# Kernel optimization log

Hardware: AMD Instinct MI355X
Metric: run time of the kernel (lower is better)

## Reference

```python
import jax, jax.numpy as jnp
import numpy as np

N_NODES = 100000
N_EDGES = 1600000
N_GRAPHS = 2000
IN_DIM, HID, OUT_DIM, N_CLS = 6, 256, 128, 60
EPS = 1e-5


def setup_inputs() -> dict:
    key = jax.random.key(0)
    ks = jax.random.split(key, 16)
    def lin(k, i, o):
        s = 1.0 / np.sqrt(i)
        k1, k2 = jax.random.split(k)
        return (jax.random.uniform(k1, (i, o), jnp.float32, -s, s),
                jax.random.uniform(k2, (o,), jnp.float32, -s, s))
    W_emb, b_emb = lin(ks[0], IN_DIM, HID)
    Wc1, bc1 = lin(ks[1], HID, HID)
    W2, b2 = lin(ks[2], HID, HID)
    Wc2, bc2 = lin(ks[3], HID, HID)
    W3, b3 = lin(ks[4], HID, OUT_DIM)
    Wcls, bcls = lin(ks[5], OUT_DIM, N_CLS)
    return {
        'node_features': jax.random.normal(ks[6], (N_NODES, IN_DIM), jnp.float32),
        'src': jax.random.randint(ks[7], (N_EDGES,), 0, N_NODES, jnp.int32),
        'dst': jax.random.randint(ks[8], (N_EDGES,), 0, N_NODES, jnp.int32),
        'graph_ids': jnp.sort(jax.random.randint(ks[9], (N_NODES,), 0, N_GRAPHS, jnp.int32)),
        'W_emb': W_emb, 'b_emb': b_emb,
        'Wc1': Wc1, 'bc1': bc1,
        'g1': jnp.ones((HID,), jnp.float32), 'be1': jnp.zeros((HID,), jnp.float32),
        'W2': W2, 'b2': b2,
        'Wc2': Wc2, 'bc2': bc2,
        'g2': jnp.ones((HID,), jnp.float32), 'be2': jnp.zeros((HID,), jnp.float32),
        'W3': W3, 'b3': b3,
        'Wcls': Wcls, 'bcls': bcls,
    }


def _graph_conv(x, W, b, src, dst, dout_isqrt, din_isqrt):
    # DGL GraphConv, norm='both': msg = x_src * dout^-1/2, sum to dst, * din^-1/2, then W, b
    m = x[src] * dout_isqrt[src][:, None]            # [E, H]
    agg = jax.ops.segment_sum(m, dst, num_segments=N_NODES)
    agg = agg * din_isqrt[:, None]
    return agg @ W + b


def _bn(h, g, b):
    # BatchNorm1d, training mode: batch stats over node dim, biased variance
    mu = jnp.mean(h, axis=0)
    var = jnp.mean(jnp.square(h - mu), axis=0)
    return (h - mu) * jax.lax.rsqrt(var + EPS) * g + b


def reference(node_features, src, dst, graph_ids, W_emb, b_emb, Wc1, bc1, g1, be1,
              W2, b2, Wc2, bc2, g2, be2, W3, b3, Wcls, bcls):
    ones_e = jnp.ones((N_EDGES,), jnp.float32)
    dout = jax.ops.segment_sum(ones_e, src, num_segments=N_NODES)
    din = jax.ops.segment_sum(ones_e, dst, num_segments=N_NODES)
    dout_isqrt = jnp.where(dout > 0, jax.lax.rsqrt(jnp.maximum(dout, 1.0)), 0.0)
    din_isqrt = jnp.where(din > 0, jax.lax.rsqrt(jnp.maximum(din, 1.0)), 0.0)

    x = node_features @ W_emb + b_emb                              # [N, H]
    h = x + _graph_conv(x, Wc1, bc1, src, dst, dout_isqrt, din_isqrt)
    h = jax.nn.relu(_bn(h, g1, be1))
    h = h @ W2 + b2
    h = x + _graph_conv(h, Wc2, bc2, src, dst, dout_isqrt, din_isqrt)
    h = jax.nn.relu(_bn(h, g2, be2))
    h = h @ W3 + b3                                                # [N, OUT_DIM]

    # dgl.mean_nodes: per-graph mean of h
    sums = jax.ops.segment_sum(h, graph_ids, num_segments=N_GRAPHS)
    cnts = jax.ops.segment_sum(jnp.ones((N_NODES,), jnp.float32), graph_ids, num_segments=N_GRAPHS)
    y = sums / jnp.maximum(cnts, 1.0)[:, None]                     # [G, OUT_DIM]
    label = y @ Wcls + bcls                                        # [G, N_CLS]
    return h, label
```

## Files before the change

kernel.cpp:

```cpp
#include <hip/hip_runtime.h>

#define NNODES 100000
#define MPAD   100032
#define NEDGES 1600000
#define NGRAPHS 2000
#define HID 256
#define OUTD 128
#define NCLS 60
#define BN_EPS 1e-5f
#define NROWBLK 1563
#define NSCANBLK 98
#define REDBLK 32

typedef __attribute__((ext_vector_type(8))) short bf16x8;
typedef __attribute__((ext_vector_type(4))) float f32x4;

__device__ __forceinline__ float b2f(unsigned short b) {
    unsigned int u = ((unsigned int)b) << 16;
    return __builtin_bit_cast(float, u);
}
__device__ __forceinline__ unsigned short f2b(float f) {
    unsigned int u = __builtin_bit_cast(unsigned int, f);
    u = (u + 0x7FFFu + ((u >> 16) & 1u)) >> 16;
    return (unsigned short)u;
}

__global__ void k_zero_int(int* __restrict__ p, int n) {
    int i = blockIdx.x * blockDim.x + threadIdx.x;
    if (i < n) p[i] = 0;
}

__global__ void k_deg(const int* __restrict__ src, const int* __restrict__ dst,
                      int* __restrict__ dout, int* __restrict__ din) {
    int e = blockIdx.x * blockDim.x + threadIdx.x;
    if (e < NEDGES) {
        atomicAdd(&dout[src[e]], 1);
        atomicAdd(&din[dst[e]], 1);
    }
}

__global__ void k_isqrt(const int* __restrict__ dout, const int* __restrict__ din,
                        float* __restrict__ dos, float* __restrict__ dis) {
    int i = blockIdx.x * blockDim.x + threadIdx.x;
    if (i < NNODES) {
        int a = dout[i], b = din[i];
        dos[i] = a > 0 ? 1.0f / sqrtf((float)a) : 0.0f;
        dis[i] = b > 0 ? 1.0f / sqrtf((float)b) : 0.0f;
    }
}

__global__ void k_blk_sum(const int* __restrict__ deg, int* __restrict__ bsum) {
    __shared__ int red[256];
    int blk = blockIdx.x, tid = threadIdx.x;
    int base = blk * 1024;
    int s = 0;
#pragma unroll
    for (int j = 0; j < 4; ++j) {
        int i = base + tid + j * 256;
        if (i < NNODES) s += deg[i];
    }
    red[tid] = s;
    __syncthreads();
    for (int off = 128; off > 0; off >>= 1) {
        if (tid < off) red[tid] += red[tid + off];
        __syncthreads();
    }
    if (tid == 0) bsum[blk] = red[0];
}

__global__ void k_scan_bsum(int* __restrict__ bsum) {
    if (threadIdx.x == 0) {
        int acc = 0;
        for (int i = 0; i < NSCANBLK; ++i) { int v = bsum[i]; bsum[i] = acc; acc += v; }
    }
}

__global__ void k_scan_local(const int* __restrict__ deg, const int* __restrict__ bsum,
                             int* __restrict__ row_ptr, int* __restrict__ cursor) {
    __shared__ int buf[1024];
    int blk = blockIdx.x, tid = threadIdx.x;
    int i = blk * 1024 + tid;
    int v = (i < NNODES) ? deg[i] : 0;
    buf[tid] = v;
    __syncthreads();
    for (int off = 1; off < 1024; off <<= 1) {
        int t = (tid >= off) ? buf[tid - off] : 0;
        __syncthreads();
        buf[tid] += t;
        __syncthreads();
    }
    int inc = buf[tid] + bsum[blk];
    if (i < NNODES) { row_ptr[i + 1] = inc; cursor[i] = inc - v; }
    if (i == 0) row_ptr[0] = 0;
}

__global__ void k_scatter(const int* __restrict__ src, const int* __restrict__ dst,
                          const float* __restrict__ dos, int* __restrict__ cursor,
                          int2* __restrict__ csr_ew) {
    int e = blockIdx.x * blockDim.x + threadIdx.x;
    if (e < NEDGES) {
        int s = src[e], d = dst[e];
        int pos = atomicAdd(&cursor[d], 1);
        csr_ew[pos] = make_int2(s, __float_as_int(dos[s]));
    }
}

__global__ void k_wconv(const float* __restrict__ W, unsigned short* __restrict__ Wt,
                        int K, int N) {
    int idx = blockIdx.x * 256 + threadIdx.x;
    if (idx >= N * K) return;
    int n = idx / K, k = idx - n * K;
    Wt[idx] = f2b(W[(size_t)k * N + n]);
}

__global__ void k_small_mm(const float* __restrict__ Wemb, const float* __restrict__ bemb,
                           const float* __restrict__ Wc1, float* __restrict__ M1,
                           float* __restrict__ v1) {
    int c = threadIdx.x;
    int bi = blockIdx.x;
    float acc = 0.f;
    if (bi < 6) {
        for (int k = 0; k < HID; ++k) acc = fmaf(Wemb[bi * HID + k], Wc1[k * HID + c], acc);
        M1[bi * HID + c] = acc;
    } else {
        for (int k = 0; k < HID; ++k) acc = fmaf(bemb[k], Wc1[k * HID + c], acc);
        v1[c] = acc;
    }
}

__global__ void k_agg6(const int* __restrict__ row_ptr, const int2* __restrict__ csr_ew,
                       const float* __restrict__ nf,
                       float* __restrict__ t6, float* __restrict__ u1) {
    int n = blockIdx.x * blockDim.x + threadIdx.x;
    if (n >= NNODES) return;
    float a0 = 0, a1 = 0, a2 = 0, a3 = 0, a4 = 0, a5 = 0, au = 0;
    int s = row_ptr[n], e = row_ptr[n + 1];
    int i = s;
    for (; i + 2 <= e; i += 2) {
        int2 g0 = csr_ew[i], g1 = csr_ew[i + 1];
        float w0 = __int_as_float(g0.y), w1 = __int_as_float(g1.y);
        const float* p0 = nf + (size_t)g0.x * 6;
        const float* p1 = nf + (size_t)g1.x * 6;
        a0 = fmaf(w0, p0[0], a0); a1 = fmaf(w0, p0[1], a1); a2 = fmaf(w0, p0[2], a2);
        a3 = fmaf(w0, p0[3], a3); a4 = fmaf(w0, p0[4], a4); a5 = fmaf(w0, p0[5], a5);
        au += w0;
        a0 = fmaf(w1, p1[0], a0); a1 = fmaf(w1, p1[1], a1); a2 = fmaf(w1, p1[2], a2);
        a3 = fmaf(w1, p1[3], a3); a4 = fmaf(w1, p1[4], a4); a5 = fmaf(w1, p1[5], a5);
        au += w1;
    }
    for (; i < e; ++i) {
        int2 g0 = csr_ew[i];
        float w = __int_as_float(g0.y);
        const float* p = nf + (size_t)g0.x * 6;
        a0 = fmaf(w, p[0], a0); a1 = fmaf(w, p[1], a1); a2 = fmaf(w, p[2], a2);
        a3 = fmaf(w, p[3], a3); a4 = fmaf(w, p[4], a4); a5 = fmaf(w, p[5], a5);
        au += w;
    }
    float* t = t6 + (size_t)n * 6;
    t[0] = a0; t[1] = a1; t[2] = a2; t[3] = a3; t[4] = a4; t[5] = a5;
    u1[n] = au;
}

__global__ __launch_bounds__(256) void k_layer1(
    const float* __restrict__ nf, const float* __restrict__ Wemb, const float* __restrict__ bemb,
    const float* __restrict__ M1, const float* __restrict__ v1, const float* __restrict__ bc1,
    const float* __restrict__ t6, const float* __restrict__ u1, const float* __restrict__ dis,
    unsigned short* __restrict__ H, float* __restrict__ psum, float* __restrict__ psq) {
    __shared__ float s_nf[64][6];
    __shared__ float s_t6[64][6];
    __shared__ float s_u[64];
    __shared__ float s_r[64];
    int blk = blockIdx.x;
    int n0 = blk * 64;
    int tid = threadIdx.x;
    for (int t = tid; t < 384; t += 256) {
        int nl = t / 6, i = t % 6;
        int n = n0 + nl;
        s_nf[nl][i] = (n < NNODES) ? nf[(size_t)n * 6 + i] : 0.f;
        s_t6[nl][i] = (n < NNODES) ? t6[(size_t)n * 6 + i] : 0.f;
    }
    if (tid < 64) {
        int n = n0 + tid;
        s_u[tid] = (n < NNODES) ? u1[n] : 0.f;
        s_r[tid] = (n < NNODES) ? dis[n] : 0.f;
    }
    int c = tid;
    float wc[6], mc[6];
#pragma unroll
    for (int i = 0; i < 6; ++i) { wc[i] = Wemb[i * HID + c]; mc[i] = M1[i * HID + c]; }
    float v1c = v1[c];
    float bsum = bemb[c] + bc1[c];
    __syncthreads();
    float ps = 0.f, pq = 0.f;
    int nmax = min(64, NNODES - n0);
    for (int nl = 0; nl < nmax; ++nl) {
        float nfd = 0.f, td = 0.f;
#pragma unroll
        for (int i = 0; i < 6; ++i) {
            nfd = fmaf(s_nf[nl][i], wc[i], nfd);
            td = fmaf(s_t6[nl][i], mc[i], td);
        }
        float val = nfd + s_r[nl] * (td + s_u[nl] * v1c) + bsum;
        H[(size_t)(n0 + nl) * HID + c] = f2b(val);
        ps += val;
        pq = fmaf(val, val, pq);
    }
    for (int nl = nmax; nl < 64; ++nl) H[(size_t)(n0 + nl) * HID + c] = 0;
    psum[blk * HID + c] = ps;
    psq[blk * HID + c] = pq;
}

__global__ void k_bn_part(const float* __restrict__ psum, const float* __restrict__ psq,
                          double* __restrict__ tmp) {
    int c = threadIdx.x;
    int s = blockIdx.x;
    double a = 0.0, b = 0.0;
    for (int bb = s; bb < NROWBLK; bb += REDBLK) {
        a += psum[bb * HID + c];
        b += psq[bb * HID + c];
    }
    tmp[s * HID + c] = a;
    tmp[(REDBLK + s) * HID + c] = b;
}

__global__ void k_bn_final(const double* __restrict__ tmp, const float* __restrict__ g,
                           const float* __restrict__ be, float* __restrict__ scale,
                           float* __restrict__ shift) {
    int c = threadIdx.x;
    double s = 0.0, q = 0.0;
    for (int i = 0; i < REDBLK; ++i) { s += tmp[i * HID + c]; q += tmp[(REDBLK + i) * HID + c]; }
    double mu = s / (double)NNODES;
    double var = q / (double)NNODES - mu * mu;
    if (var < 0.0) var = 0.0;
    double inv = 1.0 / sqrt(var + (double)BN_EPS);
    float sc = (float)((double)g[c] * inv);
    scale[c] = sc;
    shift[c] = be[c] - (float)mu * sc;
}

template <int NC, bool ATRANS, bool XEPI, bool PART, bool OUTF32>
__global__ __launch_bounds__(256, 2) void k_mgemm(
    const unsigned short* __restrict__ A, const unsigned short* __restrict__ Bt,
    const float* __restrict__ bias,
    const float* __restrict__ scale, const float* __restrict__ shift,
    const float* __restrict__ nf, const float* __restrict__ Wemb, const float* __restrict__ bemb,
    unsigned short* __restrict__ Cb, float* __restrict__ Cf,
    float* __restrict__ psum, float* __restrict__ psq) {
    __shared__ unsigned short As[64 * 256];
    __shared__ unsigned short Bs[64 * 256];
    __shared__ float sSc[HID];
    __shared__ float sSh[HID];
    __shared__ float sNf[64][6];
    __shared__ float sXW[6][HID];
    __shared__ float redS[2][64];
    __shared__ float redQ[2][64];

    int tid = threadIdx.x;
    int rb = blockIdx.x;
    int row0 = rb * 64;

    if (ATRANS) { sSc[tid] = scale[tid]; sSh[tid] = shift[tid]; }
    if (XEPI) {
        for (int t = tid; t < 6 * NC; t += 256) {
            int i = t / NC, cl = t % NC;
            sXW[i][cl] = Wemb[i * HID + cl];
        }
        if (tid < 64) {
            int n = row0 + tid;
#pragma unroll
            for (int i = 0; i < 6; ++i) sNf[tid][i] = (n < NNODES) ? nf[(size_t)n * 6 + i] : 0.f;
        }
    }
    if (ATRANS) __syncthreads();

#pragma unroll
    for (int i = 0; i < 8; ++i) {
        int g = i * 256 + tid;
        int row = g >> 5, kc = g & 31;
        uint4 v = *(const uint4*)(A + (size_t)(row0 + row) * 256 + kc * 8);
        if (ATRANS) {
            unsigned int w[4] = {v.x, v.y, v.z, v.w};
#pragma unroll
            for (int q = 0; q < 4; ++q) {
                int k0 = kc * 8 + q * 2;
                float f0 = b2f((unsigned short)(w[q] & 0xffffu));
                float f1 = b2f((unsigned short)(w[q] >> 16));
                f0 = fmaxf(fmaf(f0, sSc[k0], sSh[k0]), 0.f);
                f1 = fmaxf(fmaf(f1, sSc[k0 + 1], sSh[k0 + 1]), 0.f);
                w[q] = (unsigned int)f2b(f0) | ((unsigned int)f2b(f1) << 16);
            }
            v.x = w[0]; v.y = w[1]; v.z = w[2]; v.w = w[3];
        }
        int pkc = kc ^ (row & 7);
        *(uint4*)(&As[row * 256 + pkc * 8]) = v;
    }

    int w = tid >> 6, lane = tid & 63;
    int wm = w >> 1, wn = w & 1;
    int lrow = lane & 15, lk = lane >> 4;

    for (int cb = 0; cb < NC / 64; ++cb) {
        int c0 = cb * 64;
        if (cb) __syncthreads();
#pragma unroll
        for (int i = 0; i < 8; ++i) {
            int g = i * 256 + tid;
            int row = g >> 5, kc = g & 31;
            uint4 v = *(const uint4*)(Bt + (size_t)(c0 + row) * 256 + kc * 8);
            int pkc = kc ^ (row & 7);
            *(uint4*)(&Bs[row * 256 + pkc * 8]) = v;
        }
        __syncthreads();

        f32x4 acc[2][2] = {};
#pragma unroll
        for (int ks = 0; ks < 8; ++ks) {
            bf16x8 af[2], bfr[2];
#pragma unroll
            for (int fm = 0; fm < 2; ++fm) {
                int r = wm * 32 + fm * 16 + lrow;
                int kc = ks * 4 + lk;
                af[fm] = *(const bf16x8*)(&As[r * 256 + (kc ^ (r & 7)) * 8]);
            }
#pragma unroll
            for (int fn = 0; fn < 2; ++fn) {
                int r = wn * 32 + fn * 16 + lrow;
                int kc = ks * 4 + lk;
                bfr[fn] = *(const bf16x8*)(&Bs[r * 256 + (kc ^ (r & 7)) * 8]);
            }
#pragma unroll
            for (int fm = 0; fm < 2; ++fm)
#pragma unroll
                for (int fn = 0; fn < 2; ++fn)
                    acc[fm][fn] = __builtin_amdgcn_mfma_f32_16x16x32_bf16(af[fm], bfr[fn], acc[fm][fn], 0, 0, 0);
        }

        float pS[2] = {0.f, 0.f}, pQ[2] = {0.f, 0.f};
#pragma unroll
        for (int fn = 0; fn < 2; ++fn) {
            int cl = wn * 32 + fn * 16 + lrow;
            int gc = c0 + cl;
            float bv = bias[gc];
            if (XEPI) bv += bemb[gc];
#pragma unroll
            for (int fm = 0; fm < 2; ++fm) {
#pragma unroll
                for (int r = 0; r < 4; ++r) {
                    int rl = wm * 32 + fm * 16 + lk * 4 + r;
                    int gr = row0 + rl;
                    float val = acc[fm][fn][r] + bv;
                    if (XEPI) {
#pragma unroll
                        for (int l = 0; l < 6; ++l) val = fmaf(sNf[rl][l], sXW[l][gc], val);
                    }
                    if (gr < NNODES) {
                        if (OUTF32) Cf[(size_t)gr * NC + gc] = val;
                        else        Cb[(size_t)gr * NC + gc] = f2b(val);
                        if (PART) { pS[fn] += val; pQ[fn] = fmaf(val, val, pQ[fn]); }
                    }
                }
            }
        }
        if (PART) {
#pragma unroll
            for (int fn = 0; fn < 2; ++fn) {
                float s = pS[fn], q = pQ[fn];
                s += __shfl_xor(s, 16); s += __shfl_xor(s, 32);
                q += __shfl_xor(q, 16); q += __shfl_xor(q, 32);
                if (lk == 0) {
                    int cl = wn * 32 + fn * 16 + lrow;
                    redS[wm][cl] = s;
                    redQ[wm][cl] = q;
                }
            }
            __syncthreads();
            if (tid < 64) {
                psum[(size_t)rb * HID + c0 + tid] = redS[0][tid] + redS[1][tid];
                psq [(size_t)rb * HID + c0 + tid] = redQ[0][tid] + redQ[1][tid];
            }
        }
    }
}

__global__ __launch_bounds__(256) void k_agg(const int* __restrict__ row_ptr,
                                             const int2* __restrict__ csr_ew,
                                             const unsigned short* __restrict__ X,
                                             const float* __restrict__ dis,
                                             unsigned short* __restrict__ out) {
    int wid = threadIdx.x >> 6, lane = threadIdx.x & 63;
    int n = blockIdx.x * 4 + wid;
    if (n >= NNODES) return;
    int s = row_ptr[n], e = row_ptr[n + 1];
    float a0 = 0.f, a1 = 0.f, a2 = 0.f, a3 = 0.f;
    int i = s;
    for (; i + 4 <= e; i += 4) {
        int2 e0 = csr_ew[i], e1 = csr_ew[i + 1], e2 = csr_ew[i + 2], e3 = csr_ew[i + 3];
        uint2 v0 = ((const uint2*)(X + (size_t)e0.x * HID))[lane];
        uint2 v1 = ((const uint2*)(X + (size_t)e1.x * HID))[lane];
        uint2 v2 = ((const uint2*)(X + (size_t)e2.x * HID))[lane];
        uint2 v3 = ((const uint2*)(X + (size_t)e3.x * HID))[lane];
        float w0 = __int_as_float(e0.y), w1 = __int_as_float(e1.y);
        float w2 = __int_as_float(e2.y), w3 = __int_as_float(e3.y);
        a0 = fmaf(w0, b2f((unsigned short)(v0.x & 0xffffu)), a0);
        a1 = fmaf(w0, b2f((unsigned short)(v0.x >> 16)), a1);
        a2 = fmaf(w0, b2f((unsigned short)(v0.y & 0xffffu)), a2);
        a3 = fmaf(w0, b2f((unsigned short)(v0.y >> 16)), a3);
        a0 = fmaf(w1, b2f((unsigned short)(v1.x & 0xffffu)), a0);
        a1 = fmaf(w1, b2f((unsigned short)(v1.x >> 16)), a1);
        a2 = fmaf(w1, b2f((unsigned short)(v1.y & 0xffffu)), a2);
        a3 = fmaf(w1, b2f((unsigned short)(v1.y >> 16)), a3);
        a0 = fmaf(w2, b2f((unsigned short)(v2.x & 0xffffu)), a0);
        a1 = fmaf(w2, b2f((unsigned short)(v2.x >> 16)), a1);
        a2 = fmaf(w2, b2f((unsigned short)(v2.y & 0xffffu)), a2);
        a3 = fmaf(w2, b2f((unsigned short)(v2.y >> 16)), a3);
        a0 = fmaf(w3, b2f((unsigned short)(v3.x & 0xffffu)), a0);
        a1 = fmaf(w3, b2f((unsigned short)(v3.x >> 16)), a1);
        a2 = fmaf(w3, b2f((unsigned short)(v3.y & 0xffffu)), a2);
        a3 = fmaf(w3, b2f((unsigned short)(v3.y >> 16)), a3);
    }
    for (; i < e; ++i) {
        int2 e0 = csr_ew[i];
        float w = __int_as_float(e0.y);
        uint2 v = ((const uint2*)(X + (size_t)e0.x * HID))[lane];
        a0 = fmaf(w, b2f((unsigned short)(v.x & 0xffffu)), a0);
        a1 = fmaf(w, b2f((unsigned short)(v.x >> 16)), a1);
        a2 = fmaf(w, b2f((unsigned short)(v.y & 0xffffu)), a2);
        a3 = fmaf(w, b2f((unsigned short)(v.y >> 16)), a3);
    }
    float r = dis[n];
    ushort4 o;
    o.x = f2b(a0 * r); o.y = f2b(a1 * r); o.z = f2b(a2 * r); o.w = f2b(a3 * r);
    ((ushort4*)(out + (size_t)n * HID))[lane] = o;
}

__global__ __launch_bounds__(128) void k_mean_label(const float* __restrict__ Hout,
                                                    const int* __restrict__ gids,
                                                    const float* __restrict__ Wcls,
                                                    const float* __restrict__ bcls,
                                                    float* __restrict__ lab) {
    int g = blockIdx.x;
    int c = threadIdx.x;
    int lo = 0, hi = NNODES;
    while (lo < hi) { int mid = (lo + hi) >> 1; if (gids[mid] < g) lo = mid + 1; else hi = mid; }
    int s = lo;
    hi = NNODES;
    while (lo < hi) { int mid = (lo + hi) >> 1; if (gids[mid] < g + 1) lo = mid + 1; else hi = mid; }
    int e = lo;
    float acc = 0.f;
    for (int n = s; n < e; ++n) acc += Hout[(size_t)n * OUTD + c];
    int cnt = e - s;
    float y = acc / (float)max(cnt, 1);
    __shared__ float ys[OUTD];
    ys[c] = y;
    __syncthreads();
    if (c < NCLS) {
        float a = bcls[c];
        for (int k = 0; k < OUTD; ++k) a = fmaf(ys[k], Wcls[k * NCLS + c], a);
        lab[(size_t)g * NCLS + c] = a;
    }
}

extern "C" void kernel_launch(void* const* d_in, const int* in_sizes, int n_in,
                              void* d_out, int out_size, void* d_ws, size_t ws_size,
                              hipStream_t stream) {
    const float* nf   = (const float*)d_in[0];
    const int*   src  = (const int*)d_in[1];
    const int*   dst  = (const int*)d_in[2];
    const int*   gids = (const int*)d_in[3];
    const float* Wemb = (const float*)d_in[4];
    const float* bemb = (const float*)d_in[5];
    const float* Wc1  = (const float*)d_in[6];
    const float* bc1  = (const float*)d_in[7];
    const float* g1   = (const float*)d_in[8];
    const float* be1  = (const float*)d_in[9];
    const float* W2   = (const float*)d_in[10];
    const float* b2   = (const float*)d_in[11];
    const float* Wc2  = (const float*)d_in[12];
    const float* bc2  = (const float*)d_in[13];
    const float* g2   = (const float*)d_in[14];
    const float* be2  = (const float*)d_in[15];
    const float* W3   = (const float*)d_in[16];
    const float* b3   = (const float*)d_in[17];
    const float* Wcls = (const float*)d_in[18];
    const float* bcls = (const float*)d_in[19];

    float* out_h   = (float*)d_out;
    float* out_lab = out_h + (size_t)NNODES * OUTD;

    float* ws = (float*)d_ws;
    size_t off = 0;
    auto take = [&](size_t n) { float* p = ws + off; off += (n + 63) & ~(size_t)63; return p; };
    unsigned short* actA = (unsigned short*)take((size_t)MPAD * HID / 2);
    unsigned short* actB = (unsigned short*)take((size_t)MPAD * HID / 2);
    unsigned short* Wt2  = (unsigned short*)take(HID * HID / 2);
    unsigned short* Wtc2 = (unsigned short*)take(HID * HID / 2);
    unsigned short* Wt3  = (unsigned short*)take(OUTD * HID / 2);
    int*   deg_out = (int*)take(NNODES);
    int*   deg_in  = (int*)take(NNODES);
    float* dout_is = take(NNODES);
    float* din_is  = take(NNODES);
    int*   row_ptr = (int*)take(NNODES + 1);
    int*   cursor  = (int*)take(NNODES);
    int2*  csr_ew  = (int2*)take((size_t)NEDGES * 2);
    float* t6      = take((size_t)NNODES * 6);
    float* u1      = take(NNODES);
    float* M1      = take(6 * HID);
    float* v1      = take(HID);
    float* psum    = take((size_t)NROWBLK * HID);
    float* psq     = take((size_t)NROWBLK * HID);
    float* scale1  = take(HID);
    float* shift1  = take(HID);
    float* scale2  = take(HID);
    float* shift2  = take(HID);
    int*   bsum    = (int*)take(128);
    double* bn_tmp = (double*)take(2 * 2 * REDBLK * HID);

    k_zero_int<<<(2 * 100032 + 255) / 256, 256, 0, stream>>>(deg_out, 2 * 100032);
    k_deg<<<(NEDGES + 255) / 256, 256, 0, stream>>>(src, dst, deg_out, deg_in);
    k_isqrt<<<(NNODES + 255) / 256, 256, 0, stream>>>(deg_out, deg_in, dout_is, din_is);
    k_blk_sum<<<NSCANBLK, 256, 0, stream>>>(deg_in, bsum);
    k_scan_bsum<<<1, 64, 0, stream>>>(bsum);
    k_scan_local<<<NSCANBLK, 1024, 0, stream>>>(deg_in, bsum, row_ptr, cursor);
    k_scatter<<<(NEDGES + 255) / 256, 256, 0, stream>>>(src, dst, dout_is, cursor, csr_ew);
    k_wconv<<<(HID * HID + 255) / 256, 256, 0, stream>>>(W2, Wt2, HID, HID);
    k_wconv<<<(HID * HID + 255) / 256, 256, 0, stream>>>(Wc2, Wtc2, HID, HID);
    k_wconv<<<(HID * OUTD + 255) / 256, 256, 0, stream>>>(W3, Wt3, HID, OUTD);
    k_small_mm<<<7, 256, 0, stream>>>(Wemb, bemb, Wc1, M1, v1);
    k_agg6<<<(NNODES + 255) / 256, 256, 0, stream>>>(row_ptr, csr_ew, nf, t6, u1);
    k_layer1<<<NROWBLK, 256, 0, stream>>>(nf, Wemb, bemb, M1, v1, bc1, t6, u1, din_is,
                                          actA, psum, psq);
    k_bn_part<<<REDBLK, 256, 0, stream>>>(psum, psq, bn_tmp);
    k_bn_final<<<1, 256, 0, stream>>>(bn_tmp, g1, be1, scale1, shift1);
    k_mgemm<HID, true, false, false, false><<<NROWBLK, 256, 0, stream>>>(
        actA, Wt2, b2, scale1, shift1, nullptr, nullptr, nullptr, actB, nullptr, nullptr, nullptr);
    k_agg<<<NNODES / 4, 256, 0, stream>>>(row_ptr, csr_ew, actB, din_is, actA);
    k_mgemm<HID, false, true, true, false><<<NROWBLK, 256, 0, stream>>>(
        actA, Wtc2, bc2, nullptr, nullptr, nf, Wemb, bemb, actB, nullptr, psum, psq);
    k_bn_part<<<REDBLK, 256, 0, stream>>>(psum, psq, bn_tmp);
    k_bn_final<<<1, 256, 0, stream>>>(bn_tmp, g2, be2, scale2, shift2);
    k_mgemm<OUTD, true, false, false, true><<<NROWBLK, 256, 0, stream>>>(
        actB, Wt3, b3, scale2, shift2, nullptr, nullptr, nullptr, nullptr, out_h, nullptr, nullptr);
    k_mean_label<<<NGRAPHS, OUTD, 0, stream>>>(out_h, gids, Wcls, bcls, out_lab);
}
```

Before: 779.6 us.

## Record edge slot at degree count and widen aggregation loads to 16 bytes

The degree-counting kernel now stores the value returned by the in-degree atomic as each edge's local slot. The CSR build can then place edges at row_ptr[dst] + slot without a second pass of atomics on a cursor array. The aggregation kernel splits each wavefront into two 32-lane halves, each gathering a different neighbour row with 16-byte loads. The halves are combined with a cross-lane shuffle before one half writes the result. This trades an extra edge-length int buffer for fewer atomics and more memory parallelism in the gather.

```diff
diff --git a/kernel.cpp b/kernel.cpp
--- a/kernel.cpp
+++ b/kernel.cpp
@@ -30,12 +30,13 @@
     if (i < n) p[i] = 0;
 }
 
-__global__ void k_deg(const int* __restrict__ src, const int* __restrict__ dst,
-                      int* __restrict__ dout, int* __restrict__ din) {
+__global__ void k_deg2(const int* __restrict__ src, const int* __restrict__ dst,
+                       int* __restrict__ dout, int* __restrict__ din,
+                       int* __restrict__ lpos) {
     int e = blockIdx.x * blockDim.x + threadIdx.x;
     if (e < NEDGES) {
         atomicAdd(&dout[src[e]], 1);
-        atomicAdd(&din[dst[e]], 1);
+        lpos[e] = atomicAdd(&din[dst[e]], 1);
     }
 }
 
@@ -76,7 +77,7 @@
 }
 
 __global__ void k_scan_local(const int* __restrict__ deg, const int* __restrict__ bsum,
-                             int* __restrict__ row_ptr, int* __restrict__ cursor) {
+                             int* __restrict__ row_ptr) {
     __shared__ int buf[1024];
     int blk = blockIdx.x, tid = threadIdx.x;
     int i = blk * 1024 + tid;
@@ -90,18 +91,17 @@
         __syncthreads();
     }
     int inc = buf[tid] + bsum[blk];
-    if (i < NNODES) { row_ptr[i + 1] = inc; cursor[i] = inc - v; }
+    if (i < NNODES) row_ptr[i + 1] = inc;
     if (i == 0) row_ptr[0] = 0;
 }
 
-__global__ void k_scatter(const int* __restrict__ src, const int* __restrict__ dst,
-                          const float* __restrict__ dos, int* __restrict__ cursor,
-                          int2* __restrict__ csr_ew) {
+__global__ void k_place(const int* __restrict__ src, const int* __restrict__ dst,
+                        const int* __restrict__ lpos, const int* __restrict__ row_ptr,
+                        const float* __restrict__ dos, int2* __restrict__ csr_ew) {
     int e = blockIdx.x * blockDim.x + threadIdx.x;
     if (e < NEDGES) {
-        int s = src[e], d = dst[e];
-        int pos = atomicAdd(&cursor[d], 1);
-        csr_ew[pos] = make_int2(s, __float_as_int(dos[s]));
+        int s = src[e];
+        csr_ew[row_ptr[dst[e]] + lpos[e]] = make_int2(s, __float_as_int(dos[s]));
     }
 }
 
@@ -382,55 +382,64 @@
     }
 }
 
+#define ACC8(vv, ww) { \
+    a[0] = fmaf(ww, b2f((unsigned short)(vv.x & 0xffffu)), a[0]); \
+    a[1] = fmaf(ww, b2f((unsigned short)(vv.x >> 16)),     a[1]); \
+    a[2] = fmaf(ww, b2f((unsigned short)(vv.y & 0xffffu)), a[2]); \
+    a[3] = fmaf(ww, b2f((unsigned short)(vv.y >> 16)),     a[3]); \
+    a[4] = fmaf(ww, b2f((unsigned short)(vv.z & 0xffffu)), a[4]); \
+    a[5] = fmaf(ww, b2f((unsigned short)(vv.z >> 16)),     a[5]); \
+    a[6] = fmaf(ww, b2f((unsigned short)(vv.w & 0xffffu)), a[6]); \
+    a[7] = fmaf(ww, b2f((unsigned short)(vv.w >> 16)),     a[7]); }
+
 __global__ __launch_bounds__(256) void k_agg(const int* __restrict__ row_ptr,
                                              const int2* __restrict__ csr_ew,
                                              const unsigned short* __restrict__ X,
                                              const float* __restrict__ dis,
                                              unsigned short* __restrict__ out) {
     int wid = threadIdx.x >> 6, lane = threadIdx.x & 63;
+    int half = lane >> 5, l32 = lane & 31;
     int n = blockIdx.x * 4 + wid;
     if (n >= NNODES) return;
     int s = row_ptr[n], e = row_ptr[n + 1];
-    float a0 = 0.f, a1 = 0.f, a2 = 0.f, a3 = 0.f;
+    float a[8] = {0.f, 0.f, 0.f, 0.f, 0.f, 0.f, 0.f, 0.f};
     int i = s;
-    for (; i + 4 <= e; i += 4) {
-        int2 e0 = csr_ew[i], e1 = csr_ew[i + 1], e2 = csr_ew[i + 2], e3 = csr_ew[i + 3];
-        uint2 v0 = ((const uint2*)(X + (size_t)e0.x * HID))[lane];
-        uint2 v1 = ((const uint2*)(X + (size_t)e1.x * HID))[lane];
-        uint2 v2 = ((const uint2*)(X + (size_t)e2.x * HID))[lane];
-        uint2 v3 = ((const uint2*)(X + (size_t)e3.x * HID))[lane];
+    for (; i + 8 <= e; i += 8) {
+        int2 e0 = csr_ew[i + half];
+        int2 e1 = csr_ew[i + 2 + half];
+        int2 e2 = csr_ew[i + 4 + half];
+        int2 e3 = csr_ew[i + 6 + half];
+        uint4 v0 = ((const uint4*)(X + (size_t)e0.x * HID))[l32];
+        uint4 v1 = ((const uint4*)(X + (size_t)e1.x * HID))[l32];
+        uint4 v2 = ((const uint4*)(X + (size_t)e2.x * HID))[l32];
+        uint4 v3 = ((const uint4*)(X + (size_t)e3.x * HID))[l32];
         float w0 = __int_as_float(e0.y), w1 = __int_as_float(e1.y);
         float w2 = __int_as_float(e2.y), w3 = __int_as_float(e3.y);
-        a0 = fmaf(w0, b2f((unsigned short)(v0.x & 0xffffu)), a0);
-        a1 = fmaf(w0, b2f((unsigned short)(v0.x >> 16)), a1);
-        a2 = fmaf(w0, b2f((unsigned short)(v0.y & 0xffffu)), a2);
-        a3 = fmaf(w0, b2f((unsigned short)(v0.y >> 16)), a3);
-        a0 = fmaf(w1, b2f((unsigned short)(v1.x & 0xffffu)), a0);
-        a1 = fmaf(w1, b2f((unsigned short)(v1.x >> 16)), a1);
-        a2 = fmaf(w1, b2f((unsigned short)(v1.y & 0xffffu)), a2);
-        a3 = fmaf(w1, b2f((unsigned short)(v1.y >> 16)), a3);
-        a0 = fmaf(w2, b2f((unsigned short)(v2.x & 0xffffu)), a0);
-        a1 = fmaf(w2, b2f((unsigned short)(v2.x >> 16)), a1);
-        a2 = fmaf(w2, b2f((unsigned short)(v2.y & 0xffffu)), a2);
-        a3 = fmaf(w2, b2f((unsigned short)(v2.y >> 16)), a3);
-        a0 = fmaf(w3, b2f((unsigned short)(v3.x & 0xffffu)), a0);
-        a1 = fmaf(w3, b2f((unsigned short)(v3.x >> 16)), a1);
-        a2 = fmaf(w3, b2f((unsigned short)(v3.y & 0xffffu)), a2);
-        a3 = fmaf(w3, b2f((unsigned short)(v3.y >> 16)), a3);
-    }
-    for (; i < e; ++i) {
+        ACC8(v0, w0) ACC8(v1, w1) ACC8(v2, w2) ACC8(v3, w3)
+    }
+    for (; i + 2 <= e; i += 2) {
+        int2 e0 = csr_ew[i + half];
+        uint4 v0 = ((const uint4*)(X + (size_t)e0.x * HID))[l32];
+        float w0 = __int_as_float(e0.y);
+        ACC8(v0, w0)
+    }
+    if (i < e && half == 0) {
         int2 e0 = csr_ew[i];
-        float w = __int_as_float(e0.y);
-        uint2 v = ((const uint2*)(X + (size_t)e0.x * HID))[lane];
-        a0 = fmaf(w, b2f((unsigned short)(v.x & 0xffffu)), a0);
-        a1 = fmaf(w, b2f((unsigned short)(v.x >> 16)), a1);
-        a2 = fmaf(w, b2f((unsigned short)(v.y & 0xffffu)), a2);
-        a3 = fmaf(w, b2f((unsigned short)(v.y >> 16)), a3);
-    }
-    float r = dis[n];
-    ushort4 o;
-    o.x = f2b(a0 * r); o.y = f2b(a1 * r); o.z = f2b(a2 * r); o.w = f2b(a3 * r);
-    ((ushort4*)(out + (size_t)n * HID))[lane] = o;
+        uint4 v0 = ((const uint4*)(X + (size_t)e0.x * HID))[l32];
+        float w0 = __int_as_float(e0.y);
+        ACC8(v0, w0)
+    }
+#pragma unroll
+    for (int j = 0; j < 8; ++j) a[j] += __shfl_xor(a[j], 32);
+    if (half == 0) {
+        float r = dis[n];
+        uint4 o;
+        o.x = (unsigned)f2b(a[0] * r) | ((unsigned)f2b(a[1] * r) << 16);
+        o.y = (unsigned)f2b(a[2] * r) | ((unsigned)f2b(a[3] * r) << 16);
+        o.z = (unsigned)f2b(a[4] * r) | ((unsigned)f2b(a[5] * r) << 16);
+        o.w = (unsigned)f2b(a[6] * r) | ((unsigned)f2b(a[7] * r) << 16);
+        ((uint4*)(out + (size_t)n * HID))[l32] = o;
+    }
 }
 
 __global__ __launch_bounds__(128) void k_mean_label(const float* __restrict__ Hout,
@@ -500,7 +509,7 @@
     float* dout_is = take(NNODES);
     float* din_is  = take(NNODES);
     int*   row_ptr = (int*)take(NNODES + 1);
-    int*   cursor  = (int*)take(NNODES);
+    int*   lpos    = (int*)take(NEDGES);
     int2*  csr_ew  = (int2*)take((size_t)NEDGES * 2);
     float* t6      = take((size_t)NNODES * 6);
     float* u1      = take(NNODES);
@@ -516,12 +525,12 @@
     double* bn_tmp = (double*)take(2 * 2 * REDBLK * HID);
 
     k_zero_int<<<(2 * 100032 + 255) / 256, 256, 0, stream>>>(deg_out, 2 * 100032);
-    k_deg<<<(NEDGES + 255) / 256, 256, 0, stream>>>(src, dst, deg_out, deg_in);
+    k_deg2<<<(NEDGES + 255) / 256, 256, 0, stream>>>(src, dst, deg_out, deg_in, lpos);
     k_isqrt<<<(NNODES + 255) / 256, 256, 0, stream>>>(deg_out, deg_in, dout_is, din_is);
     k_blk_sum<<<NSCANBLK, 256, 0, stream>>>(deg_in, bsum);
     k_scan_bsum<<<1, 64, 0, stream>>>(bsum);
-    k_scan_local<<<NSCANBLK, 1024, 0, stream>>>(deg_in, bsum, row_ptr, cursor);
-    k_scatter<<<(NEDGES + 255) / 256, 256, 0, stream>>>(src, dst, dout_is, cursor, csr_ew);
+    k_scan_local<<<NSCANBLK, 1024, 0, stream>>>(deg_in, bsum, row_ptr);
+    k_place<<<(NEDGES + 255) / 256, 256, 0, stream>>>(src, dst, lpos, row_ptr, dout_is, csr_ew);
     k_wconv<<<(HID * HID + 255) / 256, 256, 0, stream>>>(W2, Wt2, HID, HID);
     k_wconv<<<(HID * HID + 255) / 256, 256, 0, stream>>>(Wc2, Wtc2, HID, HID);
     k_wconv<<<(HID * OUTD + 255) / 256, 256, 0, stream>>>(W3, Wt3, HID, OUTD);
```

Measured after the change: 724.0 us. 1.08x faster.
